# Kernel tuning notes

Hardware: AMD Instinct MI355X
Metric: run time of the kernel (lower is better)

The kernel has to match this reference:

```python
import jax, jax.numpy as jnp
import numpy as np

B, T, D, H = 4, 2048, 1152, 8
HD = D // H          # 144
ROT = HD             # full rotary
SCALE = HD ** -0.5


def _rotate_half(x):
    # x: [..., ROT]
    x1, x2 = x[..., : ROT // 2], x[..., ROT // 2 :]
    return jnp.concatenate([-x2, x1], axis=-1)


def _apply_rotary(q, k, cos, sin):
    # q,k: [B,H,T,HD]; cos,sin: [T,ROT] broadcast over B,H
    q_rot, q_pass = q[..., :ROT], q[..., ROT:]
    k_rot, k_pass = k[..., :ROT], k[..., ROT:]
    q = jnp.concatenate([q_rot * cos + _rotate_half(q_rot) * sin, q_pass], axis=-1)
    k = jnp.concatenate([k_rot * cos + _rotate_half(k_rot) * sin, k_pass], axis=-1)
    return q, k


def setup_inputs() -> dict:
    key = jax.random.key(0)
    ks = jax.random.split(key, 7)
    init = 1.0 / np.sqrt(D)  # keep activations well-scaled
    return {
        "x": jax.random.normal(ks[0], (B, T, D), dtype=jnp.float32),
        "cos": jax.random.uniform(ks[1], (T, ROT), dtype=jnp.float32),
        "sin": jax.random.uniform(ks[2], (T, ROT), dtype=jnp.float32),
        "Wq": jax.random.normal(ks[3], (D, D), dtype=jnp.float32) * init,
        "Wk": jax.random.normal(ks[4], (D, D), dtype=jnp.float32) * init,
        "Wv": jax.random.normal(ks[5], (D, D), dtype=jnp.float32) * init,
        "Wo": jax.random.normal(ks[6], (D, D), dtype=jnp.float32) * init,
    }


def reference(x, cos, sin, Wq, Wk, Wv, Wo):
    # nn.Linear(bias=False): y = x @ W.T
    def proj(W):
        y = jnp.einsum("btd,ed->bte", x, W)
        return y.reshape(B, T, H, HD).transpose(0, 2, 1, 3)  # [B,H,T,HD]

    q, k, v = proj(Wq), proj(Wk), proj(Wv)
    q, k = _apply_rotary(q, k, cos, sin)
    scores = jnp.einsum("bhqd,bhkd->bhqk", q, k) * SCALE
    attn = jax.nn.softmax(scores, axis=-1)
    o = jnp.einsum("bhqk,bhkd->bhqd", attn, v)
    o = o.transpose(0, 2, 1, 3).reshape(B, T, D)
    return jnp.einsum("btd,ed->bte", o, Wo)
```

## Files before the change

kernel.cpp:

```cpp
#include <hip/hip_runtime.h>
#include <cstdint>
#include <cstddef>

typedef __bf16 bf16;
typedef bf16 bf16x8 __attribute__((ext_vector_type(8)));
typedef bf16 bf16x4 __attribute__((ext_vector_type(4)));
typedef bf16 bf16x2 __attribute__((ext_vector_type(2)));
typedef float f32x4 __attribute__((ext_vector_type(4)));
typedef float f32x16 __attribute__((ext_vector_type(16)));
typedef uint32_t u32x2 __attribute__((ext_vector_type(2)));
typedef uint32_t u32x4 __attribute__((ext_vector_type(4)));

#define DEVI __device__ __forceinline__

#define CB 4
#define CT 2048
#define CD 1152
#define CH 8
#define CHD 144
#define CBT 8192

constexpr int GTBUF = 128 * 40;

DEVI void gload_lds16(const void* g, void* l) {
  __builtin_amdgcn_global_load_lds(
      (const __attribute__((address_space(1))) void*)g,
      (__attribute__((address_space(3))) void*)l, 16, 0, 0);
}

DEVI f32x4 mfma16(bf16x8 a, bf16x8 b, f32x4 c) {
  return __builtin_amdgcn_mfma_f32_16x16x32_bf16(a, b, c, 0, 0, 0);
}
DEVI f32x16 mfma32(bf16x8 a, bf16x8 b, f32x16 c) {
  return __builtin_amdgcn_mfma_f32_32x32x16_bf16(a, b, c, 0, 0, 0);
}

DEVI uint32_t cvtpk(float lo, float hi) {
  uint32_t r;
  asm("v_cvt_pk_bf16_f32 %0, %1, %2" : "=v"(r) : "v"(lo), "v"(hi));
  return r;
}

DEVI f32x16 zero16() {
  f32x16 z;
#pragma unroll
  for (int i = 0; i < 16; ++i) z[i] = 0.f;
  return z;
}

__global__ __launch_bounds__(256) void k_cast(const float* __restrict__ in,
                                              bf16* __restrict__ out, int n8) {
  int i = blockIdx.x * 256 + threadIdx.x;
  if (i >= n8) return;
  const float4* p = (const float4*)in + (size_t)i * 2;
  float4 a = p[0], b = p[1];
  bf16x8 o;
  o[0] = (bf16)a.x; o[1] = (bf16)a.y; o[2] = (bf16)a.z; o[3] = (bf16)a.w;
  o[4] = (bf16)b.x; o[5] = (bf16)b.y; o[6] = (bf16)b.z; o[7] = (bf16)b.w;
  ((bf16x8*)out)[i] = o;
}

__global__ __launch_bounds__(256) void k_cast4(
    const float* __restrict__ a, const float* __restrict__ b,
    const float* __restrict__ c, const float* __restrict__ d,
    bf16* __restrict__ oa, bf16* __restrict__ ob,
    bf16* __restrict__ oc, bf16* __restrict__ od, int n8) {
  int w = blockIdx.y;
  const float* in = (w == 0) ? a : (w == 1) ? b : (w == 2) ? c : d;
  bf16* out = (w == 0) ? oa : (w == 1) ? ob : (w == 2) ? oc : od;
  int i = blockIdx.x * 256 + threadIdx.x;
  if (i >= n8) return;
  const float4* p = (const float4*)in + (size_t)i * 2;
  float4 x = p[0], y = p[1];
  bf16x8 o;
  o[0] = (bf16)x.x; o[1] = (bf16)x.y; o[2] = (bf16)x.z; o[3] = (bf16)x.w;
  o[4] = (bf16)y.x; o[5] = (bf16)y.y; o[6] = (bf16)y.z; o[7] = (bf16)y.w;
  int oi = i;
  if (w < 2) {
    int e = i / 144, ch = i - e * 144;
    int h2 = e / CHD, j = e - h2 * CHD;
    int ep = h2 * CHD + ((j < 72) ? (2 * j) : (2 * (j - 72) + 1));
    oi = ep * 144 + ch;
  }
  ((bf16x8*)out)[oi] = o;
}

__global__ __launch_bounds__(256) void k_csbuild(const float* __restrict__ cosb,
                                                 const float* __restrict__ sinb,
                                                 float2* __restrict__ cst) {
  int i = blockIdx.x * 256 + threadIdx.x;
  int t = i / CHD, s = i - t * CHD;
  int p = s >> 1;
  float2 v;
  if (s & 1) {
    v.x = cosb[(size_t)t * CHD + 72 + p];
    v.y = sinb[(size_t)t * CHD + 72 + p];
  } else {
    v.x = cosb[(size_t)t * CHD + p];
    v.y = -sinb[(size_t)t * CHD + p];
  }
  cst[i] = v;
}

template <int MODE>
DEVI void gemm_body(bf16* __restrict__ smem,
                    const bf16* __restrict__ A, const bf16* __restrict__ W,
                    void* __restrict__ Cout, int bm0, int bn0, float scl,
                    const float2* __restrict__ cst) {
  constexpr int K = CD, N = CD;
  bf16* As = smem;
  bf16* Bs = smem + 2 * GTBUF;
  const int tid = threadIdx.x;
  const int lane = tid & 63, wid = tid >> 6;
  const int l15 = lane & 15, g = lane >> 4;
  const int wm = wid >> 1, wn = wid & 1;

  const bf16* asrc[3];
  const bf16* wsrc[3];
  int ldo[3];
  bool on[3];
#pragma unroll
  for (int c = 0; c < 3; ++c) {
    int li = tid + (c << 8);
    on[c] = (li < 640);
    int li2 = on[c] ? li : 0;
    int e0 = li2 << 3;
    int row = e0 / 40, col = e0 % 40;
    if (col >= 32) col = 24;
    asrc[c] = &A[(size_t)(bm0 + row) * K + col];
    wsrc[c] = &W[(size_t)(bn0 + row) * K + col];
    ldo[c] = (li2 & ~63) * 8;
  }

#define G_STAGE(k0, buf)                                                     \
  do {                                                                       \
    bf16* Ad = As + (buf)*GTBUF;                                             \
    bf16* Bd = Bs + (buf)*GTBUF;                                             \
    _Pragma("unroll") for (int c = 0; c < 3; ++c) if (on[c]) {               \
      gload_lds16(asrc[c] + (k0), Ad + ldo[c]);                              \
      gload_lds16(wsrc[c] + (k0), Bd + ldo[c]);                              \
    }                                                                        \
  } while (0)

  f32x4 acc[4][4];
  for (int mi = 0; mi < 4; ++mi)
    for (int ni = 0; ni < 4; ++ni) {
      acc[mi][ni][0] = 0.f; acc[mi][ni][1] = 0.f;
      acc[mi][ni][2] = 0.f; acc[mi][ni][3] = 0.f;
    }

  const int nk = K >> 5;
  G_STAGE(0, 0);
  __syncthreads();

  int cur = 0;
  for (int kt = 0; kt < nk; ++kt) {
    if (kt + 1 < nk) G_STAGE((kt + 1) << 5, cur ^ 1);
    __builtin_amdgcn_sched_barrier(0);

    const bf16* Ac = As + cur * GTBUF;
    const bf16* Bc = Bs + cur * GTBUF;
    bf16x8 af[4], bfr[4];
    for (int mi = 0; mi < 4; ++mi)
      af[mi] = *(const bf16x8*)&Ac[(wm * 64 + mi * 16 + l15) * 40 + g * 8];
    for (int ni = 0; ni < 4; ++ni)
      bfr[ni] = *(const bf16x8*)&Bc[(wn * 64 + ni * 16 + l15) * 40 + g * 8];
    __builtin_amdgcn_s_setprio(1);
    for (int mi = 0; mi < 4; ++mi)
      for (int ni = 0; ni < 4; ++ni)
        acc[mi][ni] = mfma16(af[mi], bfr[ni], acc[mi][ni]);
    __builtin_amdgcn_s_setprio(0);
    __syncthreads();
    cur ^= 1;
  }
#undef G_STAGE

  if (MODE == 0) {
    for (int ni = 0; ni < 4; ++ni) {
      int colg = bn0 + wn * 64 + ni * 16 + l15;
      int s = colg % CHD;
      for (int mi = 0; mi < 4; ++mi)
        for (int r = 0; r < 4; ++r) {
          int rowg = bm0 + wm * 64 + mi * 16 + g * 4 + r;
          int tloc = rowg & (CT - 1);
          float2 cs = cst[(size_t)tloc * CHD + s];
          float own = acc[mi][ni][r];
          float oth = __shfl_xor(own, 1);
          ((bf16*)Cout)[(size_t)rowg * N + colg] =
              (bf16)((own * cs.x + oth * cs.y) * scl);
        }
    }
  } else if (MODE == 1) {
    for (int ni = 0; ni < 4; ++ni) {
      int colg = bn0 + wn * 64 + ni * 16 + l15;
      int h2 = colg / CHD, hd = colg - h2 * CHD;
      for (int mi = 0; mi < 4; ++mi) {
        int rowg0 = bm0 + wm * 64 + mi * 16 + g * 4;
        int b2 = rowg0 >> 11;
        int t = rowg0 & (CT - 1);
        bf16x4 w4;
        for (int r = 0; r < 4; ++r) w4[r] = (bf16)acc[mi][ni][r];
        *(bf16x4*)&((bf16*)Cout)[((size_t)((b2 * CH + h2) * CHD + hd)) * CT + t] = w4;
      }
    }
  } else {
    for (int mi = 0; mi < 4; ++mi)
      for (int ni = 0; ni < 4; ++ni)
        for (int r = 0; r < 4; ++r) {
          int rowg = bm0 + wm * 64 + mi * 16 + g * 4 + r;
          int colg = bn0 + wn * 64 + ni * 16 + l15;
          ((float*)Cout)[(size_t)rowg * N + colg] = acc[mi][ni][r];
        }
  }
}

__global__ __launch_bounds__(256) void k_gemm_qkv(
    const bf16* __restrict__ A, const bf16* __restrict__ Wq,
    const bf16* __restrict__ Wk, const bf16* __restrict__ Wv,
    bf16* __restrict__ q, bf16* __restrict__ k, bf16* __restrict__ vT,
    const float2* __restrict__ cst) {
  __shared__ __align__(16) bf16 smem[4 * GTBUF];
  const int nx = gridDim.x, ny = gridDim.y;
  const int nwg = nx * ny * gridDim.z;
  const int orig = (blockIdx.z * ny + blockIdx.y) * nx + blockIdx.x;
  const int logical = (orig & 7) * (nwg >> 3) + (orig >> 3);
  const int lx = logical % nx;
  const int rest = logical / nx;
  const int ly = rest % ny, lz = rest / ny;
  if (lz == 0)
    gemm_body<0>(smem, A, Wq, q, ly * 128, lx * 128, 0.120224587f, cst);
  else if (lz == 1)
    gemm_body<0>(smem, A, Wk, k, ly * 128, lx * 128, 1.0f, cst);
  else
    gemm_body<1>(smem, A, Wv, vT, ly * 128, lx * 128, 0.f, cst);
}

__global__ __launch_bounds__(256) void k_gemm_out(
    const bf16* __restrict__ A, const bf16* __restrict__ W, float* __restrict__ out) {
  __shared__ __align__(16) bf16 smem[4 * GTBUF];
  const int nx = gridDim.x, ny = gridDim.y;
  const int nwg = nx * ny;
  const int orig = blockIdx.y * nx + blockIdx.x;
  const int logical = (orig & 7) * (nwg >> 3) + (orig >> 3);
  const int lx = logical % nx, ly = logical / nx;
  gemm_body<2>(smem, A, W, out, ly * 128, lx * 128, 0.f, nullptr);
}

DEVI void build_pfrag(const f32x16& s, float m, bf16x8& f0, bf16x8& f1) {
  uint32_t pk[8];
#pragma unroll
  for (int a = 0; a < 8; ++a) {
    float p0 = exp2f(s[2 * a] - m);
    float p1 = exp2f(s[2 * a + 1] - m);
    pk[a] = cvtpk(p0, p1);
  }
  u32x2 r02 = __builtin_amdgcn_permlane32_swap(pk[0], pk[2], false, false);
  u32x2 r13 = __builtin_amdgcn_permlane32_swap(pk[1], pk[3], false, false);
  u32x2 r46 = __builtin_amdgcn_permlane32_swap(pk[4], pk[6], false, false);
  u32x2 r57 = __builtin_amdgcn_permlane32_swap(pk[5], pk[7], false, false);
  u32x4 w0 = {r02[0], r13[0], r02[1], r13[1]};
  u32x4 w1 = {r46[0], r57[0], r46[1], r57[1]};
  f0 = __builtin_bit_cast(bf16x8, w0);
  f1 = __builtin_bit_cast(bf16x8, w1);
}

DEVI float max32(const f32x16& s0, const f32x16& s1) {
  float q0 = fmaxf(fmaxf(s0[0], s0[1]), fmaxf(s0[2], s0[3]));
  float q1 = fmaxf(fmaxf(s0[4], s0[5]), fmaxf(s0[6], s0[7]));
  float q2 = fmaxf(fmaxf(s0[8], s0[9]), fmaxf(s0[10], s0[11]));
  float q3 = fmaxf(fmaxf(s0[12], s0[13]), fmaxf(s0[14], s0[15]));
  float q4 = fmaxf(fmaxf(s1[0], s1[1]), fmaxf(s1[2], s1[3]));
  float q5 = fmaxf(fmaxf(s1[4], s1[5]), fmaxf(s1[6], s1[7]));
  float q6 = fmaxf(fmaxf(s1[8], s1[9]), fmaxf(s1[10], s1[11]));
  float q7 = fmaxf(fmaxf(s1[12], s1[13]), fmaxf(s1[14], s1[15]));
  return fmaxf(fmaxf(fmaxf(q0, q1), fmaxf(q2, q3)),
               fmaxf(fmaxf(q4, q5), fmaxf(q6, q7)));
}

__global__ __launch_bounds__(256, 2) void k_attn(const bf16* __restrict__ qg,
                                                 const bf16* __restrict__ kg,
                                                 const bf16* __restrict__ vT,
                                                 bf16* __restrict__ og) {
  const int lin = blockIdx.x;
  const int xcd = lin & 7, idx = lin >> 3;
  const int bh = ((idx & 3) << 3) | xcd;
  const int qx = idx >> 2;
  const int b = bh >> 3, h = bh & 7;
  const int q0 = qx << 7;
  const int tid = threadIdx.x, lane = tid & 63, wq = tid >> 6;
  const int l31 = lane & 31, hi = lane >> 5;
  const int hi16 = hi * 16;
  const int kx7 = l31 & 7;
  const int kxor = kx7 << 4;

  constexpr int KBUF = 64 * 144;
  constexpr int VBUF = 160 * 64;
  __shared__ __align__(16) bf16 Ks[2 * KBUF];
  __shared__ __align__(16) bf16 Vs[2 * VBUF];

  bf16x8 qf[9];
  {
    const bf16* qbase = qg + (size_t)(b * CT + q0 + wq * 32 + l31) * CD + h * CHD + hi * 8;
#pragma unroll
    for (int ks = 0; ks < 9; ++ks) qf[ks] = *(const bf16x8*)&qbase[ks * 16];
  }

  const bf16* ksrc[5];
  const bf16* vsrc[5];
  int kldo[5], vldo[5];
#pragma unroll
  for (int it = 0; it < 5; ++it) {
    int c = tid + it * 256;
    if (c >= 1152) c = 0;
    int krow = c / 18, kj = c - krow * 18;
    int kgr = (kj < 16) ? (kj ^ (krow & 7)) : kj;
    ksrc[it] = kg + (size_t)(b * CT + krow) * CD + h * CHD + kgr * 8;
    kldo[it] = (c & ~63) * 8;
    int vr = c >> 3, vj = c & 7;
    int vgr = vj ^ (vr & 7);
    vsrc[it] = vT + (size_t)(bh * CHD + vr) * CT + vgr * 8;
    vldo[it] = (c & ~63) * 8;
  }

  {
    int bsel = tid >> 7, off = tid & 127;
    int row = 144 + (off >> 3), cj = off & 7;
    uint32_t one2 = 0x3F803F80u;
    u32x4 val;
    if (row == 144) { val[0] = one2; val[1] = one2; val[2] = one2; val[3] = one2; }
    else { val[0] = 0u; val[1] = 0u; val[2] = 0u; val[3] = 0u; }
    *(u32x4*)(Vs + bsel * VBUF + row * 64 + cj * 8) = val;
  }

#define STAGE_TILE(kv, buf)                                                 \
  do {                                                                      \
    bf16* Kn = Ks + (buf)*KBUF;                                             \
    bf16* Vn = Vs + (buf)*VBUF;                                             \
    _Pragma("unroll") for (int it = 0; it < 4; ++it) {                      \
      gload_lds16(ksrc[it] + (size_t)(kv)*CD, Kn + kldo[it]);               \
      gload_lds16(vsrc[it] + (kv), Vn + vldo[it]);                          \
    }                                                                       \
    if (tid < 128) {                                                        \
      gload_lds16(ksrc[4] + (size_t)(kv)*CD, Kn + kldo[4]);                 \
      gload_lds16(vsrc[4] + (kv), Vn + vldo[4]);                            \
    }                                                                       \
  } while (0)

  STAGE_TILE(0, 0);
  __syncthreads();

  f32x16 oacc[5];
#pragma unroll
  for (int u = 0; u < 5; ++u) oacc[u] = zero16();
  float mrow = -__builtin_inff();

  int cur = 0;
  for (int t = 0; t < 32; ++t) {
    bf16* Kc = Ks + cur * KBUF;
    bf16* Vc = Vs + cur * VBUF;

    if (t < 31) STAGE_TILE((t + 1) << 6, cur ^ 1);
    __builtin_amdgcn_sched_barrier(0);

    const char* kr0 = (const char*)Kc + (size_t)l31 * 288;
    const char* kr1 = kr0 + 32 * 288;
    f32x16 s0 = zero16(), s1 = zero16();
    __builtin_amdgcn_s_setprio(1);
#pragma unroll
    for (int ks = 0; ks < 9; ++ks) {
      int cc = 2 * ks + hi;
      int off = ((ks < 8) ? (cc ^ kx7) : cc) << 4;
      s0 = mfma32(*(const bf16x8*)(kr0 + off), qf[ks], s0);
      s1 = mfma32(*(const bf16x8*)(kr1 + off), qf[ks], s1);
    }
    __builtin_amdgcn_s_setprio(0);

    float mt = max32(s0, s1);
    mt = fmaxf(mt, __shfl_xor(mt, 32));

    if (mt > mrow + 8.0f) {
      float alpha = exp2f(mrow - mt);
#pragma unroll
      for (int u = 0; u < 5; ++u) oacc[u] = oacc[u] * alpha;
      mrow = mt;
    }

    bf16x8 pf0, pf1, pf2, pf3;
    build_pfrag(s0, mrow, pf0, pf1);
    build_pfrag(s1, mrow, pf2, pf3);

    __builtin_amdgcn_s_setprio(1);
#pragma unroll
    for (int u = 0; u < 5; ++u) {
      const char* vrow = (const char*)Vc + (size_t)(u * 32 + l31) * 128;
      oacc[u] = mfma32(*(const bf16x8*)(vrow + ((0 * 32 + hi16) ^ kxor)), pf0, oacc[u]);
      oacc[u] = mfma32(*(const bf16x8*)(vrow + ((1 * 32 + hi16) ^ kxor)), pf1, oacc[u]);
      oacc[u] = mfma32(*(const bf16x8*)(vrow + ((2 * 32 + hi16) ^ kxor)), pf2, oacc[u]);
      oacc[u] = mfma32(*(const bf16x8*)(vrow + ((3 * 32 + hi16) ^ kxor)), pf3, oacc[u]);
    }
    __builtin_amdgcn_s_setprio(0);

    __syncthreads();
    cur ^= 1;
  }
#undef STAGE_TILE

  float ls = oacc[4][8];
  float lo = __shfl_xor(ls, 32);
  if (hi) ls = lo;
  float inv = 1.0f / ls;

  bf16* ob = og + (size_t)(b * CT + q0 + wq * 32 + l31) * CD + h * CHD;
#pragma unroll
  for (int u = 0; u < 5; ++u) {
#pragma unroll
    for (int pr = 0; pr < 8; ++pr) {
      if (u == 4 && pr >= 4) continue;
      int hd = u * 32 + ((2 * pr) & 3) + 8 * (pr >> 1) + 4 * hi;
      bf16x2 w;
      w[0] = (bf16)(oacc[u][2 * pr] * inv);
      w[1] = (bf16)(oacc[u][2 * pr + 1] * inv);
      *(bf16x2*)&ob[hd] = w;
    }
  }
}

extern "C" void kernel_launch(void* const* d_in, const int* in_sizes, int n_in,
                              void* d_out, int out_size, void* d_ws, size_t ws_size,
                              hipStream_t stream) {
  const float* x = (const float*)d_in[0];
  const float* cosb = (const float*)d_in[1];
  const float* sinb = (const float*)d_in[2];
  const float* Wq = (const float*)d_in[3];
  const float* Wk = (const float*)d_in[4];
  const float* Wv = (const float*)d_in[5];
  const float* Wo = (const float*)d_in[6];

  char* ws = (char*)d_ws;
  bf16* xb   = (bf16*)(ws + 0);
  bf16* wqb  = (bf16*)(ws + 18874368);
  bf16* wkb  = (bf16*)(ws + 21528576);
  bf16* wvb  = (bf16*)(ws + 24182784);
  bf16* wob  = (bf16*)(ws + 26836992);
  bf16* qlin = (bf16*)(ws + 29491200);
  bf16* klin = (bf16*)(ws + 48365568);
  bf16* vT   = (bf16*)(ws + 67239936);
  float2* cst = (float2*)(ws + 86114304);

  k_cast<<<4608, 256, 0, stream>>>(x, xb, CBT * CD / 8);
  k_cast4<<<dim3(648, 4), 256, 0, stream>>>(Wq, Wk, Wv, Wo, wqb, wkb, wvb, wob,
                                            CD * CD / 8);
  k_csbuild<<<1152, 256, 0, stream>>>(cosb, sinb, cst);

  k_gemm_qkv<<<dim3(CD / 128, CBT / 128, 3), 256, 0, stream>>>(
      xb, wqb, wkb, wvb, qlin, klin, vT, cst);
  k_attn<<<512, 256, 0, stream>>>(qlin, klin, vT, xb);
  k_gemm_out<<<dim3(CD / 128, CBT / 128), 256, 0, stream>>>(xb, wob, (float*)d_out);
}
```

Measured before the change: 254.6 us.

## Enlarge GEMM tiles to 256x128 with 512 threads and XOR-swizzled LDS

Both projection GEMMs now use a 256x128 output tile computed by 8 waves of 512 threads, instead of 128x128 with 4 waves. Each W tile is therefore reused across twice as many A rows, which cuts global/L2 traffic per FLOP and halves the workgroup count. The padded 40-element LDS row stride is replaced by a dense 32-element stride with an XOR swizzle on 16-byte chunks. This removes the padding and the predicated load lanes while still avoiding bank conflicts. The cost is fewer workgroups, which lowers occupancy and worsens tail balance on a large-CU GPU, plus a larger LDS footprint per block.

```diff
diff --git a/kernel.cpp b/kernel.cpp
--- a/kernel.cpp
+++ b/kernel.cpp
@@ -20,7 +20,8 @@
 #define CHD 144
 #define CBT 8192
 
-constexpr int GTBUF = 128 * 40;
+constexpr int ABUF = 256 * 32;
+constexpr int BBUF = 128 * 32;
 
 DEVI void gload_lds16(const void* g, void* l) {
   __builtin_amdgcn_global_load_lds(
@@ -109,37 +110,38 @@
                     const float2* __restrict__ cst) {
   constexpr int K = CD, N = CD;
   bf16* As = smem;
-  bf16* Bs = smem + 2 * GTBUF;
+  bf16* Bs = smem + 2 * ABUF;
   const int tid = threadIdx.x;
   const int lane = tid & 63, wid = tid >> 6;
   const int l15 = lane & 15, g = lane >> 4;
   const int wm = wid >> 1, wn = wid & 1;
 
-  const bf16* asrc[3];
-  const bf16* wsrc[3];
-  int ldo[3];
-  bool on[3];
-#pragma unroll
-  for (int c = 0; c < 3; ++c) {
-    int li = tid + (c << 8);
-    on[c] = (li < 640);
-    int li2 = on[c] ? li : 0;
-    int e0 = li2 << 3;
-    int row = e0 / 40, col = e0 % 40;
-    if (col >= 32) col = 24;
-    asrc[c] = &A[(size_t)(bm0 + row) * K + col];
-    wsrc[c] = &W[(size_t)(bn0 + row) * K + col];
-    ldo[c] = (li2 & ~63) * 8;
+  const bf16* src0;
+  const bf16* src1;
+  const bf16* srcB;
+  int do0, do1, doB;
+  {
+    int c0 = tid;
+    int r0 = c0 >> 2, j0 = c0 & 3;
+    src0 = &A[(size_t)(bm0 + r0) * K + ((j0 ^ (r0 & 3)) << 3)];
+    do0 = (c0 & ~63) * 8;
+    int c1 = tid + 512;
+    int r1 = c1 >> 2, j1 = c1 & 3;
+    src1 = &A[(size_t)(bm0 + r1) * K + ((j1 ^ (r1 & 3)) << 3)];
+    do1 = (c1 & ~63) * 8;
+    int cb = tid;
+    int rb = cb >> 2, jb = cb & 3;
+    srcB = &W[(size_t)(bn0 + rb) * K + ((jb ^ (rb & 3)) << 3)];
+    doB = (cb & ~63) * 8;
   }
 
 #define G_STAGE(k0, buf)                                                     \
   do {                                                                       \
-    bf16* Ad = As + (buf)*GTBUF;                                             \
-    bf16* Bd = Bs + (buf)*GTBUF;                                             \
-    _Pragma("unroll") for (int c = 0; c < 3; ++c) if (on[c]) {               \
-      gload_lds16(asrc[c] + (k0), Ad + ldo[c]);                              \
-      gload_lds16(wsrc[c] + (k0), Bd + ldo[c]);                              \
-    }                                                                        \
+    bf16* Ad = As + (buf)*ABUF;                                              \
+    bf16* Bd = Bs + (buf)*BBUF;                                              \
+    gload_lds16(src0 + (k0), Ad + do0);                                      \
+    gload_lds16(src1 + (k0), Ad + do1);                                      \
+    gload_lds16(srcB + (k0), Bd + doB);                                      \
   } while (0)
 
   f32x4 acc[4][4];
@@ -158,13 +160,17 @@
     if (kt + 1 < nk) G_STAGE((kt + 1) << 5, cur ^ 1);
     __builtin_amdgcn_sched_barrier(0);
 
-    const bf16* Ac = As + cur * GTBUF;
-    const bf16* Bc = Bs + cur * GTBUF;
+    const bf16* Ac = As + cur * ABUF;
+    const bf16* Bc = Bs + cur * BBUF;
     bf16x8 af[4], bfr[4];
-    for (int mi = 0; mi < 4; ++mi)
-      af[mi] = *(const bf16x8*)&Ac[(wm * 64 + mi * 16 + l15) * 40 + g * 8];
-    for (int ni = 0; ni < 4; ++ni)
-      bfr[ni] = *(const bf16x8*)&Bc[(wn * 64 + ni * 16 + l15) * 40 + g * 8];
+    for (int mi = 0; mi < 4; ++mi) {
+      int row = wm * 64 + mi * 16 + l15;
+      af[mi] = *(const bf16x8*)&Ac[row * 32 + ((g ^ (row & 3)) << 3)];
+    }
+    for (int ni = 0; ni < 4; ++ni) {
+      int row = wn * 64 + ni * 16 + l15;
+      bfr[ni] = *(const bf16x8*)&Bc[row * 32 + ((g ^ (row & 3)) << 3)];
+    }
     __builtin_amdgcn_s_setprio(1);
     for (int mi = 0; mi < 4; ++mi)
       for (int ni = 0; ni < 4; ++ni)
@@ -214,12 +220,12 @@
   }
 }
 
-__global__ __launch_bounds__(256) void k_gemm_qkv(
+__global__ __launch_bounds__(512) void k_gemm_qkv(
     const bf16* __restrict__ A, const bf16* __restrict__ Wq,
     const bf16* __restrict__ Wk, const bf16* __restrict__ Wv,
     bf16* __restrict__ q, bf16* __restrict__ k, bf16* __restrict__ vT,
     const float2* __restrict__ cst) {
-  __shared__ __align__(16) bf16 smem[4 * GTBUF];
+  __shared__ __align__(16) bf16 smem[2 * ABUF + 2 * BBUF];
   const int nx = gridDim.x, ny = gridDim.y;
   const int nwg = nx * ny * gridDim.z;
   const int orig = (blockIdx.z * ny + blockIdx.y) * nx + blockIdx.x;
@@ -228,22 +234,22 @@
   const int rest = logical / nx;
   const int ly = rest % ny, lz = rest / ny;
   if (lz == 0)
-    gemm_body<0>(smem, A, Wq, q, ly * 128, lx * 128, 0.120224587f, cst);
+    gemm_body<0>(smem, A, Wq, q, ly * 256, lx * 128, 0.120224587f, cst);
   else if (lz == 1)
-    gemm_body<0>(smem, A, Wk, k, ly * 128, lx * 128, 1.0f, cst);
+    gemm_body<0>(smem, A, Wk, k, ly * 256, lx * 128, 1.0f, cst);
   else
-    gemm_body<1>(smem, A, Wv, vT, ly * 128, lx * 128, 0.f, cst);
-}
-
-__global__ __launch_bounds__(256) void k_gemm_out(
+    gemm_body<1>(smem, A, Wv, vT, ly * 256, lx * 128, 0.f, cst);
+}
+
+__global__ __launch_bounds__(512) void k_gemm_out(
     const bf16* __restrict__ A, const bf16* __restrict__ W, float* __restrict__ out) {
-  __shared__ __align__(16) bf16 smem[4 * GTBUF];
+  __shared__ __align__(16) bf16 smem[2 * ABUF + 2 * BBUF];
   const int nx = gridDim.x, ny = gridDim.y;
   const int nwg = nx * ny;
   const int orig = blockIdx.y * nx + blockIdx.x;
   const int logical = (orig & 7) * (nwg >> 3) + (orig >> 3);
   const int lx = logical % nx, ly = logical / nx;
-  gemm_body<2>(smem, A, W, out, ly * 128, lx * 128, 0.f, nullptr);
+  gemm_body<2>(smem, A, W, out, ly * 256, lx * 128, 0.f, nullptr);
 }
 
 DEVI void build_pfrag(const f32x16& s, float m, bf16x8& f0, bf16x8& f1) {
@@ -452,8 +458,8 @@
                                             CD * CD / 8);
   k_csbuild<<<1152, 256, 0, stream>>>(cosb, sinb, cst);
 
-  k_gemm_qkv<<<dim3(CD / 128, CBT / 128, 3), 256, 0, stream>>>(
+  k_gemm_qkv<<<dim3(CD / 128, CBT / 256, 3), 512, 0, stream>>>(
       xb, wqb, wkb, wvb, qlin, klin, vT, cst);
   k_attn<<<512, 256, 0, stream>>>(qlin, klin, vT, xb);
-  k_gemm_out<<<dim3(CD / 128, CBT / 128), 256, 0, stream>>>(xb, wob, (float*)d_out);
-}
+  k_gemm_out<<<dim3(CD / 128, CBT / 256), 512, 0, stream>>>(xb, wob, (float*)d_out);
+}
```

New measurement: 260.9 us. 2.5% more time.
